# Performance work log

Measured on AMD Instinct MI355X. Metric: run time of the kernel, lower is better.

The kernel has to match this reference:

```python
import jax, jax.numpy as jnp
import numpy as np

TOPK = 32  # module init arg


def setup_inputs() -> dict:
    key = jax.random.key(0)
    kq, kk, kv = jax.random.split(key, 3)
    B, T, S, H, E = 1, 2048, 2048, 16, 64
    return {
        "query": jax.random.normal(kq, (B, T, H, E), dtype=jnp.float32),
        "key": jax.random.normal(kk, (B, S, H, E), dtype=jnp.float32),
        "value": jax.random.normal(kv, (B, S, H, E), dtype=jnp.float32),
    }


def reference(query, key, value):
    B, T, H, E = query.shape
    S = key.shape[1]
    softmax_temp = 1.0 / np.sqrt(E)  # default: 1/sqrt(d_keys)
    topk = min(TOPK, S)

    q = query * jnp.asarray(softmax_temp, query.dtype)
    # full dense scores, as in the original module: [B, H, T, S]
    QK = jnp.einsum('bthe,bshe->bhts', q, key)

    # oracle top-k along keys; scatter True at top-k positions (exact mask semantics)
    _, topk_idx = jax.lax.top_k(QK, topk)  # [B, H, T, k]
    keep = jnp.put_along_axis(
        jnp.zeros(QK.shape, dtype=jnp.bool_), topk_idx, True, axis=-1,
        inplace=False,
    )
    QK = jnp.where(keep, QK, -jnp.inf)

    attn = jax.nn.softmax(QK, axis=-1)  # dropout p=0.0 -> identity
    output = jnp.einsum('bhts,bshd->bthd', attn, value)
    return output
```

## Files before the change

kernel.cpp:

```cpp
#include <hip/hip_runtime.h>
#include <stdint.h>


#define T_DIM 2048
#define S_DIM 2048
#define H_DIM 16
#define E_DIM 64
#define K_TOP 32
#define TT 8
#define NWAVE 8

typedef float v2f __attribute__((ext_vector_type(2)));

__device__ __forceinline__ v2f pk_fma(v2f a, v2f b, v2f c) {
    return __builtin_elementwise_fma(a, b, c);
}

__device__ __forceinline__ unsigned f2ord(float f) {
    unsigned b = __float_as_uint(f);
    return (b & 0x80000000u) ? ~b : (b | 0x80000000u);
}
__device__ __forceinline__ float ord2f(unsigned u) {
    unsigned b = (u & 0x80000000u) ? (u ^ 0x80000000u) : ~u;
    return __uint_as_float(b);
}

__global__ __launch_bounds__(256)
void transpose_k(const float* __restrict__ Kg, float* __restrict__ KT) {
    __shared__ float tile[64][65];
    const int tid = threadIdx.x;
    const int h   = blockIdx.x & (H_DIM - 1);
    const int sb  = (blockIdx.x >> 4) * 64;
    #pragma unroll
    for (int sw = 0; sw < 4; sw++) {
        int r = sw * 16 + (tid >> 4);
        int c = (tid & 15) * 4;
        float4 v = *(const float4*)(Kg + ((size_t)(sb + r) * H_DIM + h) * E_DIM + c);
        tile[r][c] = v.x; tile[r][c+1] = v.y; tile[r][c+2] = v.z; tile[r][c+3] = v.w;
    }
    __syncthreads();
    #pragma unroll
    for (int sw = 0; sw < 4; sw++) {
        int e = sw * 16 + (tid >> 4);
        int j = (tid & 15) * 4;
        float4 v = { tile[j][e], tile[j+1][e], tile[j+2][e], tile[j+3][e] };
        *(float4*)(KT + ((size_t)h * E_DIM + e) * S_DIM + sb + j) = v;
    }
}

__global__ __launch_bounds__(512, 2)
void topk_attn_kernel(const float* __restrict__ Qg,
                      const float* __restrict__ KT,
                      const float* __restrict__ Vg,
                      float* __restrict__ Out) {
    __shared__ __align__(16) float sS[TT][S_DIM];
    __shared__ unsigned candU[NWAVE][64];
    __shared__ int      candI[NWAVE][64];
    __shared__ unsigned wcnt[NWAVE];

    const int tid  = threadIdx.x;
    const int lane = tid & 63;
    const int wv   = tid >> 6;
    const int bx   = blockIdx.x;
    const int h    = bx & (H_DIM - 1);
    const int tb   = bx >> 4;
    const int t0   = tb * TT;

    v2f acc2[TT][2];
    #pragma unroll
    for (int t = 0; t < TT; t++) { acc2[t][0] = (v2f)(0.f); acc2[t][1] = (v2f)(0.f); }

    const int   sb  = wv * 256 + (lane << 2);
    const float* kp = KT + (size_t)h * E_DIM * S_DIM + sb;
    const float* Qb = Qg + ((size_t)t0 * H_DIM + h) * E_DIM;

    float4 k0q = *(const float4*)(kp);
    float4 k1q = *(const float4*)(kp + S_DIM);
    for (int e2 = 0; e2 < 32; e2++) {
        const int ep = (e2 + 1) & 31;
        float4 n0q = *(const float4*)(kp + (size_t)(2 * ep)     * S_DIM);
        float4 n1q = *(const float4*)(kp + (size_t)(2 * ep + 1) * S_DIM);
        v2f k0lo = {k0q.x, k0q.y}, k0hi = {k0q.z, k0q.w};
        v2f k1lo = {k1q.x, k1q.y}, k1hi = {k1q.z, k1q.w};
        #pragma unroll
        for (int t = 0; t < TT; t++) {
            float2 qv = *(const float2*)(Qb + (size_t)t * (H_DIM * E_DIM) + 2 * e2);
            v2f qx = {qv.x, qv.x}, qy = {qv.y, qv.y};
            acc2[t][0] = pk_fma(qx, k0lo, acc2[t][0]);
            acc2[t][1] = pk_fma(qx, k0hi, acc2[t][1]);
            acc2[t][0] = pk_fma(qy, k1lo, acc2[t][0]);
            acc2[t][1] = pk_fma(qy, k1hi, acc2[t][1]);
        }
        k0q = n0q; k1q = n1q;
    }

    #pragma unroll
    for (int r = 0; r < TT; r++) {
        float4 f4 = { acc2[r][0].x, acc2[r][0].y, acc2[r][1].x, acc2[r][1].y };
        *(float4*)(&sS[r][sb]) = f4;
    }
    __syncthreads();

    unsigned u[32];
    #pragma unroll
    for (int i = 0; i < 32; i++) u[i] = f2ord(sS[wv][i * 64 + lane]);

    auto wave_count = [&](unsigned t) -> int {
        int c = 0;
        #pragma unroll
        for (int i = 0; i < 32; i++)
            c += __popcll(__ballot(u[i] >= t));
        return c;
    };

    unsigned thr = 0xC1800000u;
    int c = wave_count(thr);
    if (c < K_TOP || c > 64) {
        unsigned lo = (c >= K_TOP) ? thr : 0u;
        unsigned hi = (c >= K_TOP) ? 0xFFFFFFFFu : thr;
        bool found = false;
        while (!found && (hi - lo > 1u)) {
            unsigned mid = lo + ((hi - lo) >> 1);
            int cm = wave_count(mid);
            if (cm >= K_TOP && cm <= 64) { thr = mid; c = cm; found = true; }
            else if (cm >= K_TOP) lo = mid;
            else hi = mid;
        }
        if (!found) { thr = lo; c = wave_count(lo); }
    }
    int n = (c > 64) ? 64 : c;

    if (lane == 0) wcnt[wv] = 0u;
    #pragma unroll
    for (int i = 0; i < 32; i++) {
        if (u[i] >= thr) {
            unsigned pos = atomicAdd(&wcnt[wv], 1u);
            if (pos < 64u) {
                candU[wv][pos] = u[i];
                candI[wv][pos] = i * 64 + lane;
            }
        }
    }

    unsigned long long key = 0ull;
    if (lane < n)
        key = (((unsigned long long)candU[wv][lane]) << 32)
            | (unsigned)(~candI[wv][lane]);
    #pragma unroll
    for (int k = 2; k <= 64; k <<= 1)
        #pragma unroll
        for (int j = k >> 1; j > 0; j >>= 1) {
            unsigned long long ok = __shfl_xor(key, j);
            bool takemax = ((lane & j) == 0) ^ ((lane & k) != 0);
            bool mineG   = key > ok;
            key = (takemax == mineG) ? key : ok;
        }

    const float* Vb = Vg + (size_t)h * E_DIM;
    float val  = ord2f((unsigned)(key >> 32)) * 0.125f;
    int   sidx = (int)(~(unsigned)key);
    float m = __shfl(val, 0);
    float w = (lane < K_TOP) ? expf(val - m) : 0.f;
    float Z = w;
    #pragma unroll
    for (int d = 32; d > 0; d >>= 1) Z += __shfl_xor(Z, d);
    float pr = w / Z;

    float o = 0.f;
    #pragma unroll
    for (int i2 = 0; i2 < K_TOP; i2++) {
        float pi = __shfl(pr, i2);
        int   s2 = __shfl(sidx, i2);
        o = fmaf(pi, Vb[(size_t)s2 * (H_DIM * E_DIM) + lane], o);
    }
    int t = t0 + wv;
    Out[((size_t)t * H_DIM + h) * E_DIM + lane] = o;
}

extern "C" void kernel_launch(void* const* d_in, const int* in_sizes, int n_in,
                              void* d_out, int out_size, void* d_ws, size_t ws_size,
                              hipStream_t stream) {
    const float* Q = (const float*)d_in[0];
    const float* K = (const float*)d_in[1];
    const float* V = (const float*)d_in[2];
    float* O  = (float*)d_out;
    float* KT = (float*)d_ws;
    (void)in_sizes; (void)n_in; (void)out_size; (void)ws_size;
    transpose_k<<<dim3(H_DIM * (S_DIM / 64)), dim3(256), 0, stream>>>(K, KT);
    topk_attn_kernel<<<dim3((T_DIM / TT) * H_DIM), dim3(512), 0, stream>>>(Q, KT, V, O);
}
```

Measured before the change: 231.9 us.

## Use 16-bit ordered score keys in LDS for top-k threshold search

Scores are written to shared memory as the upper 16 bits of their order-preserving integer keys rather than as full floats. This halves the LDS footprint and the per-wave register array used for the ballot-based threshold search, and caps the binary search at 16 steps. Once a threshold is chosen, the owning threads re-derive full 32-bit keys from their accumulator registers and push candidates into per-row lists with atomics, which adds extra barriers. Many scores share the same 16-bit prefix, so the candidate count near the threshold can exceed 64, which risks dropping true top-k entries.

```diff
diff --git a/kernel.cpp b/kernel.cpp
--- a/kernel.cpp
+++ b/kernel.cpp
@@ -53,10 +53,11 @@
                       const float* __restrict__ KT,
                       const float* __restrict__ Vg,
                       float* __restrict__ Out) {
-    __shared__ __align__(16) float sS[TT][S_DIM];
-    __shared__ unsigned candU[NWAVE][64];
-    __shared__ int      candI[NWAVE][64];
-    __shared__ unsigned wcnt[NWAVE];
+    __shared__ __align__(16) unsigned short sU[TT][S_DIM];
+    __shared__ unsigned candU[TT][64];
+    __shared__ int      candI[TT][64];
+    __shared__ unsigned wcnt[TT];
+    __shared__ unsigned thrA[TT];
 
     const int tid  = threadIdx.x;
     const int lane = tid & 63;
@@ -96,51 +97,73 @@
 
     #pragma unroll
     for (int r = 0; r < TT; r++) {
-        float4 f4 = { acc2[r][0].x, acc2[r][0].y, acc2[r][1].x, acc2[r][1].y };
-        *(float4*)(&sS[r][sb]) = f4;
-    }
-    __syncthreads();
-
-    unsigned u[32];
-    #pragma unroll
-    for (int i = 0; i < 32; i++) u[i] = f2ord(sS[wv][i * 64 + lane]);
-
-    auto wave_count = [&](unsigned t) -> int {
+        unsigned a = f2ord(acc2[r][0].x) >> 16;
+        unsigned b = f2ord(acc2[r][0].y) >> 16;
+        unsigned c = f2ord(acc2[r][1].x) >> 16;
+        unsigned d = f2ord(acc2[r][1].y) >> 16;
+        uint2 pk; pk.x = a | (b << 16); pk.y = c | (d << 16);
+        *(uint2*)(&sU[r][sb]) = pk;
+    }
+    if (lane == 0) wcnt[wv] = 0u;
+    __syncthreads();
+
+    unsigned pk16[16];
+    {
+        const unsigned* rowp = (const unsigned*)(&sU[wv][0]);
+        #pragma unroll
+        for (int j = 0; j < 16; j++) pk16[j] = rowp[j * 64 + lane];
+    }
+    auto count16 = [&](unsigned t) -> int {
         int c = 0;
         #pragma unroll
-        for (int i = 0; i < 32; i++)
-            c += __popcll(__ballot(u[i] >= t));
+        for (int j = 0; j < 16; j++) {
+            c += __popcll(__ballot((pk16[j] & 0xFFFFu) >= t));
+            c += __popcll(__ballot((pk16[j] >> 16) >= t));
+        }
         return c;
     };
 
-    unsigned thr = 0xC1800000u;
-    int c = wave_count(thr);
+    unsigned thr = 0xC180u;
+    int c = count16(thr);
     if (c < K_TOP || c > 64) {
         unsigned lo = (c >= K_TOP) ? thr : 0u;
-        unsigned hi = (c >= K_TOP) ? 0xFFFFFFFFu : thr;
+        unsigned hi = (c >= K_TOP) ? 0x10000u : thr;
         bool found = false;
         while (!found && (hi - lo > 1u)) {
             unsigned mid = lo + ((hi - lo) >> 1);
-            int cm = wave_count(mid);
+            int cm = count16(mid);
             if (cm >= K_TOP && cm <= 64) { thr = mid; c = cm; found = true; }
             else if (cm >= K_TOP) lo = mid;
             else hi = mid;
         }
-        if (!found) { thr = lo; c = wave_count(lo); }
-    }
-    int n = (c > 64) ? 64 : c;
-
-    if (lane == 0) wcnt[wv] = 0u;
-    #pragma unroll
-    for (int i = 0; i < 32; i++) {
-        if (u[i] >= thr) {
-            unsigned pos = atomicAdd(&wcnt[wv], 1u);
-            if (pos < 64u) {
-                candU[wv][pos] = u[i];
-                candI[wv][pos] = i * 64 + lane;
+        if (!found) { thr = lo; c = count16(lo); }
+    }
+    if (lane == 0) thrA[wv] = thr;
+    __syncthreads();
+
+    #pragma unroll
+    for (int r = 0; r < TT; r++) {
+        unsigned tr = thrA[r];
+        unsigned uu0 = f2ord(acc2[r][0].x);
+        unsigned uu1 = f2ord(acc2[r][0].y);
+        unsigned uu2 = f2ord(acc2[r][1].x);
+        unsigned uu3 = f2ord(acc2[r][1].y);
+        unsigned uu[4] = {uu0, uu1, uu2, uu3};
+        #pragma unroll
+        for (int q = 0; q < 4; q++) {
+            if ((uu[q] >> 16) >= tr) {
+                unsigned pos = atomicAdd(&wcnt[r], 1u);
+                if (pos < 64u) {
+                    candU[r][pos] = uu[q];
+                    candI[r][pos] = sb + q;
+                }
             }
         }
     }
+    __syncthreads();
+
+    unsigned nw = wcnt[wv];
+    int n = (nw > 64u) ? 64 : (int)nw;
 
     unsigned long long key = 0ull;
     if (lane < n)
```

Measured after the change: 221.0 us, median of 2. 4.7% less time.
